# Optimization experiments

Hardware: AMD Instinct MI355X
Metric: run time of the kernel (lower is better)

Reference implementation:

```python
import jax, jax.numpy as jnp
import numpy as np


def setup_inputs() -> dict:
    key = jax.random.key(0)
    ks = jax.random.split(key, 6)
    B, T, Din, Dout = 128, 512, 256, 512
    s0 = 1.0 / np.sqrt(Din + Dout)
    s1 = 1.0 / np.sqrt(Dout + Dout)
    return {
        "x": jax.random.normal(ks[0], (B, T, Din), dtype=jnp.float32),
        "W_zr0": jax.random.normal(ks[1], (Din + Dout, 2 * Dout), dtype=jnp.float32) * s0,
        "b_zr0": jnp.zeros((2 * Dout,), dtype=jnp.float32),
        "W_h0": jax.random.normal(ks[2], (Din + Dout, Dout), dtype=jnp.float32) * s0,
        "b_h0": jnp.zeros((Dout,), dtype=jnp.float32),
        "W_zr1": jax.random.normal(ks[3], (Dout + Dout, 2 * Dout), dtype=jnp.float32) * s1,
        "b_zr1": jnp.zeros((2 * Dout,), dtype=jnp.float32),
        "W_h1": jax.random.normal(ks[4], (Dout + Dout, Dout), dtype=jnp.float32) * s1,
        "b_h1": jnp.zeros((Dout,), dtype=jnp.float32),
    }


def _gru_layer(x_seq, W_zr, b_zr, W_h, b_h):
    # x_seq: [B, T, D_in]; returns [B, T, D_out]
    hidden_dim = W_h.shape[1]

    def step(state, xt):
        ins = jnp.concatenate([xt, state], axis=-1)
        zr = jax.nn.sigmoid(ins @ W_zr + b_zr)
        z, r = jnp.split(zr, 2, axis=-1)
        cand_in = jnp.concatenate([xt, z * state], axis=-1)
        h_tmp = jnp.tanh(cand_in @ W_h + b_h)
        h = r * state + (1.0 - r) * h_tmp
        return h, h

    h0 = jnp.zeros((x_seq.shape[0], hidden_dim), dtype=x_seq.dtype)
    _, ys = jax.lax.scan(step, h0, jnp.swapaxes(x_seq, 0, 1))  # scan over time
    return jnp.swapaxes(ys, 0, 1)


def reference(x, W_zr0, b_zr0, W_h0, b_h0, W_zr1, b_zr1, W_h1, b_h1):
    h = _gru_layer(x, W_zr0, b_zr0, W_h0, b_h0)
    h = _gru_layer(h, W_zr1, b_zr1, W_h1, b_h1)
    return h
```

## Files before the change

kernel.cpp:

```cpp
#include <hip/hip_runtime.h>

#define NB 128
#define NT 512
#define DIN 256
#define DD 512

using bf16x8 = __attribute__((ext_vector_type(8))) short;
using f32x4v = __attribute__((ext_vector_type(4))) float;
using u32x4  = __attribute__((ext_vector_type(4))) unsigned int;

__device__ __forceinline__ unsigned short f2bf(float f) {
  unsigned int u = __builtin_bit_cast(unsigned int, f);
  u = (u + 0x7fffu + ((u >> 16) & 1u)) >> 16;
  return (unsigned short)u;
}
__device__ __forceinline__ float bf2f(unsigned short h) {
  unsigned int u = ((unsigned int)h) << 16;
  return __builtin_bit_cast(float, u);
}
__device__ __forceinline__ unsigned int packf(float v) {
  unsigned short hi = f2bf(v);
  unsigned short lo = f2bf(v - bf2f(hi));
  return (((unsigned int)hi) << 16) | lo;
}

__global__ void prep_kernel(const float* __restrict__ x, unsigned int* __restrict__ x_pk,
                            unsigned int* __restrict__ hp, unsigned int* __restrict__ cnt) {
  long i = (long)blockIdx.x * blockDim.x + threadIdx.x;
  const long stride = (long)gridDim.x * blockDim.x;
  const long NX = (long)NB * NT * DIN;
  for (long j = i; j < NX; j += stride) x_pk[j] = packf(x[j]);
  const long NH = 2L * 2 * NB * DD;
  for (long j = i; j < NH; j += stride) hp[j] = 0u;
  if (i < 4096) cnt[i] = 0u;
}

__device__ __forceinline__ void unpack16(const u32x4& q0, const u32x4& q1,
                                         bf16x8& hi, bf16x8& lo) {
  #pragma unroll
  for (int j = 0; j < 4; ++j) {
    hi[j]     = (short)(q0[j] >> 16);
    lo[j]     = (short)(q0[j] & 0xffffu);
    hi[4 + j] = (short)(q1[j] >> 16);
    lo[4 + j] = (short)(q1[j] & 0xffffu);
  }
}

template<int KN>
__device__ __forceinline__ void gemm_pk(const unsigned int* __restrict__ a,
                                        const unsigned short* __restrict__ b,
                                        int quad, f32x4v& cH0, f32x4v& cL0,
                                        f32x4v& cH1, f32x4v& cL1) {
  const unsigned int* ap = a + quad * 8;
  const unsigned short* bp = b + quad * 8;
  #pragma unroll
  for (int kk = 0; kk < KN; kk += 64) {
    u32x4 q0 = *(const u32x4*)(ap + kk);
    u32x4 q1 = *(const u32x4*)(ap + kk + 4);
    u32x4 q2 = *(const u32x4*)(ap + kk + 32);
    u32x4 q3 = *(const u32x4*)(ap + kk + 36);
    bf16x8 a0h, a0l, a1h, a1l;
    unpack16(q0, q1, a0h, a0l);
    unpack16(q2, q3, a1h, a1l);
    bf16x8 b0 = *(const bf16x8*)(bp + kk);
    bf16x8 b1 = *(const bf16x8*)(bp + kk + 32);
    cH0 = __builtin_amdgcn_mfma_f32_16x16x32_bf16(a0h, b0, cH0, 0, 0, 0);
    cL0 = __builtin_amdgcn_mfma_f32_16x16x32_bf16(a0l, b0, cL0, 0, 0, 0);
    cH1 = __builtin_amdgcn_mfma_f32_16x16x32_bf16(a1h, b1, cH1, 0, 0, 0);
    cL1 = __builtin_amdgcn_mfma_f32_16x16x32_bf16(a1l, b1, cL1, 0, 0, 0);
  }
}

template<int KN>
__device__ __forceinline__ void gemm_pk2(const unsigned int* __restrict__ a,
                                         const unsigned short* __restrict__ b0,
                                         const unsigned short* __restrict__ b1,
                                         int quad,
                                         f32x4v& zH0, f32x4v& zL0, f32x4v& zH1, f32x4v& zL1,
                                         f32x4v& rH0, f32x4v& rL0, f32x4v& rH1, f32x4v& rL1) {
  const unsigned int* ap = a + quad * 8;
  const unsigned short* b0p = b0 + quad * 8;
  const unsigned short* b1p = b1 + quad * 8;
  #pragma unroll
  for (int kk = 0; kk < KN; kk += 64) {
    u32x4 q0 = *(const u32x4*)(ap + kk);
    u32x4 q1 = *(const u32x4*)(ap + kk + 4);
    u32x4 q2 = *(const u32x4*)(ap + kk + 32);
    u32x4 q3 = *(const u32x4*)(ap + kk + 36);
    bf16x8 a0h, a0l, a1h, a1l;
    unpack16(q0, q1, a0h, a0l);
    unpack16(q2, q3, a1h, a1l);
    bf16x8 bz0 = *(const bf16x8*)(b0p + kk);
    bf16x8 bz1 = *(const bf16x8*)(b0p + kk + 32);
    bf16x8 br0 = *(const bf16x8*)(b1p + kk);
    bf16x8 br1 = *(const bf16x8*)(b1p + kk + 32);
    zH0 = __builtin_amdgcn_mfma_f32_16x16x32_bf16(a0h, bz0, zH0, 0, 0, 0);
    zL0 = __builtin_amdgcn_mfma_f32_16x16x32_bf16(a0l, bz0, zL0, 0, 0, 0);
    rH0 = __builtin_amdgcn_mfma_f32_16x16x32_bf16(a0h, br0, rH0, 0, 0, 0);
    rL0 = __builtin_amdgcn_mfma_f32_16x16x32_bf16(a0l, br0, rL0, 0, 0, 0);
    zH1 = __builtin_amdgcn_mfma_f32_16x16x32_bf16(a1h, bz1, zH1, 0, 0, 0);
    zL1 = __builtin_amdgcn_mfma_f32_16x16x32_bf16(a1l, bz1, zL1, 0, 0, 0);
    rH1 = __builtin_amdgcn_mfma_f32_16x16x32_bf16(a1h, br1, rH1, 0, 0, 0);
    rL1 = __builtin_amdgcn_mfma_f32_16x16x32_bf16(a1l, br1, rL1, 0, 0, 0);
  }
}

__device__ __forceinline__ void gbarrier(unsigned int* gf, int slot, int w, int lane,
                                         unsigned int rnd) {
  __syncthreads();
  if (threadIdx.x == 0)
    __hip_atomic_store(gf + slot * 16, rnd, __ATOMIC_RELAXED, __HIP_MEMORY_SCOPE_AGENT);
  if (w == 0) {
    for (;;) {
      unsigned int v = __hip_atomic_load(gf + lane * 16, __ATOMIC_RELAXED,
                                         __HIP_MEMORY_SCOPE_AGENT);
      if (__all((int)(v >= rnd))) break;
      __builtin_amdgcn_s_sleep(1);
    }
    if (lane == 0)
      (void)__hip_atomic_load(gf, __ATOMIC_ACQUIRE, __HIP_MEMORY_SCOPE_AGENT);
  }
  __syncthreads();
}

__global__ void __launch_bounds__(256, 1) gru_kernel(
    const float* __restrict__ Wzr0, const float* __restrict__ bzr0,
    const float* __restrict__ Wh0,  const float* __restrict__ bh0,
    const float* __restrict__ Wzr1, const float* __restrict__ bzr1,
    const float* __restrict__ Wh1,  const float* __restrict__ bh1,
    const unsigned int* __restrict__ x_pk, unsigned int* __restrict__ hp,
    unsigned int* __restrict__ zs, unsigned int* __restrict__ cnt,
    float* __restrict__ out)
{
  extern __shared__ __align__(16) unsigned char smem[];
  const int bid = blockIdx.x, tid = threadIdx.x;
  const int w = tid >> 6, lane = tid & 63, quad = lane >> 4, l16 = lane & 15;
  const int l  = bid >> 7;
  const int rb = (bid >> 5) & 3;
  const int cb = bid & 31;
  const int r0 = rb << 5;
  const int c0 = cb << 4;
  const int K  = l ? 1024 : 768;
  const int KI = l ? 512 : 256;
  const int ldw = K + 8;

  unsigned short* wlds = (unsigned short*)smem;
  float* s_lds = (float*)(smem + ((48 * ldw * 2 + 15) & ~15));
  float* r_lds = s_lds + 512;
  float* pscr  = r_lds + 512;

  const float* Wzr = l ? Wzr1 : Wzr0;
  const float* Wh  = l ? Wh1 : Wh0;
  for (int idx = tid; idx < 16 * K; idx += 256) {
    int j = idx / K, k = idx - j * K;
    wlds[j * ldw + k]        = f2bf(Wzr[k * (2 * DD) + c0 + j]);
    wlds[(16 + j) * ldw + k] = f2bf(Wzr[k * (2 * DD) + DD + c0 + j]);
    wlds[(32 + j) * ldw + k] = f2bf(Wh[k * DD + c0 + j]);
  }
  for (int idx = tid; idx < 512; idx += 256) s_lds[idx] = 0.f;
  const float bz = (l ? bzr1 : bzr0)[c0 + l16];
  const float br = (l ? bzr1 : bzr0)[DD + c0 + l16];
  const float bh = (l ? bh1 : bh0)[c0 + l16];
  __syncthreads();

  unsigned int* gf = cnt + rb * 1024;
  const int slot = l * 32 + cb;
  unsigned int rnd = 0;

  for (int s = 0; s <= NT; ++s) {
    const int p  = (s + 1) & 1;
    const int pw = s & 1;
    const bool act = l ? (s >= 1) : (s < NT);
    const int t = l ? (s - 1) : s;

    if (act) {
      const int rowHalf = w >> 1, seg = w & 1;
      const int gRow = r0 + (rowHalf << 4) + l16;
      f32x4v zH0 = {0,0,0,0}, zL0 = {0,0,0,0}, zH1 = {0,0,0,0}, zL1 = {0,0,0,0};
      f32x4v rH0 = {0,0,0,0}, rL0 = {0,0,0,0}, rH1 = {0,0,0,0}, rL1 = {0,0,0,0};
      const unsigned short* bzseg = wlds + l16 * ldw;
      const unsigned short* brseg = wlds + (16 + l16) * ldw;
      if (l == 0) {
        if (seg == 0) {
          const unsigned int* xa = x_pk + ((long)gRow * NT + t) * DIN;
          gemm_pk2<256>(xa, bzseg, brseg, quad, zH0, zL0, zH1, zL1, rH0, rL0, rH1, rL1);
        } else {
          const unsigned int* ha = hp + ((p * 2 + 0) * NB + gRow) * DD;
          gemm_pk2<512>(ha, bzseg + 256, brseg + 256, quad,
                        zH0, zL0, zH1, zL1, rH0, rL0, rH1, rL1);
        }
      } else {
        if (seg == 0) {
          const unsigned int* h0a = hp + ((p * 2 + 0) * NB + gRow) * DD;
          gemm_pk2<512>(h0a, bzseg, brseg, quad, zH0, zL0, zH1, zL1, rH0, rL0, rH1, rL1);
        } else {
          const unsigned int* h1a = hp + ((p * 2 + 1) * NB + gRow) * DD;
          gemm_pk2<512>(h1a, bzseg + 512, brseg + 512, quad,
                        zH0, zL0, zH1, zL1, rH0, rL0, rH1, rL1);
        }
      }
      float zt[4], rt[4];
      #pragma unroll
      for (int i = 0; i < 4; ++i) {
        zt[i] = (zH0[i] + zL0[i]) + (zH1[i] + zL1[i]);
        rt[i] = (rH0[i] + rL0[i]) + (rH1[i] + rL1[i]);
      }
      if (seg == 1) {
        #pragma unroll
        for (int i = 0; i < 4; ++i) {
          pscr[rowHalf * 512 + ((quad << 2) + i) * 16 + l16]       = zt[i];
          pscr[rowHalf * 512 + 256 + ((quad << 2) + i) * 16 + l16] = rt[i];
        }
      }
      __syncthreads();
      if (seg == 0) {
        #pragma unroll
        for (int i = 0; i < 4; ++i) {
          int rloc = (rowHalf << 4) + (quad << 2) + i;
          float zpre = zt[i] + pscr[rowHalf * 512 + ((quad << 2) + i) * 16 + l16] + bz;
          float rpre = rt[i] + pscr[rowHalf * 512 + 256 + ((quad << 2) + i) * 16 + l16] + br;
          float zg = 1.f / (1.f + __expf(-zpre));
          float rg = 1.f / (1.f + __expf(-rpre));
          float sv = s_lds[rloc * 16 + l16];
          __hip_atomic_store(&zs[((long)l * NB + r0 + rloc) * DD + c0 + l16],
                             packf(zg * sv), __ATOMIC_RELAXED, __HIP_MEMORY_SCOPE_AGENT);
          r_lds[rloc * 16 + l16] = rg;
        }
      }
    }
    ++rnd;
    gbarrier(gf, slot, w, lane, rnd);

    if (act) {
      const int rowHalf = w & 1, src = w >> 1;
      const int gRow = r0 + (rowHalf << 4) + l16;
      f32x4v cH0 = {0,0,0,0}, cL0 = {0,0,0,0}, cH1 = {0,0,0,0}, cL1 = {0,0,0,0};
      const unsigned short* hseg = wlds + (32 + l16) * ldw;
      if (src == 0) {
        if (l == 0) {
          const unsigned int* xa = x_pk + ((long)gRow * NT + t) * DIN;
          gemm_pk<256>(xa, hseg, quad, cH0, cL0, cH1, cL1);
        } else {
          const unsigned int* h0a = hp + ((p * 2 + 0) * NB + gRow) * DD;
          gemm_pk<512>(h0a, hseg, quad, cH0, cL0, cH1, cL1);
        }
      } else {
        const unsigned int* za = zs + ((long)l * NB + gRow) * DD;
        gemm_pk<512>(za, hseg + KI, quad, cH0, cL0, cH1, cL1);
      }
      f32x4v tot;
      #pragma unroll
      for (int i = 0; i < 4; ++i) tot[i] = (cH0[i] + cL0[i]) + (cH1[i] + cL1[i]);
      if (src == 1) {
        #pragma unroll
        for (int i = 0; i < 4; ++i)
          pscr[rowHalf * 256 + ((quad << 2) + i) * 16 + l16] = tot[i];
      }
      __syncthreads();
      if (src == 0) {
        #pragma unroll
        for (int i = 0; i < 4; ++i) {
          int rloc = (rowHalf << 4) + (quad << 2) + i;
          float pre = tot[i] + pscr[rowHalf * 256 + ((quad << 2) + i) * 16 + l16] + bh;
          float ax = fabsf(pre), e = __expf(-2.f * ax);
          float th = (1.f - e) / (1.f + e);
          th = (pre < 0.f) ? -th : th;
          float rv = r_lds[rloc * 16 + l16];
          float sv = s_lds[rloc * 16 + l16];
          float h = rv * sv + (1.f - rv) * th;
          s_lds[rloc * 16 + l16] = h;
          __hip_atomic_store(&hp[((pw * 2 + l) * NB + r0 + rloc) * DD + c0 + l16],
                             packf(h), __ATOMIC_RELAXED, __HIP_MEMORY_SCOPE_AGENT);
          if (l) out[((long)(r0 + rloc) * NT + t) * DD + c0 + l16] = h;
        }
      }
    }
    ++rnd;
    gbarrier(gf, slot, w, lane, rnd);
  }
}

extern "C" void kernel_launch(void* const* d_in, const int* in_sizes, int n_in,
                              void* d_out, int out_size, void* d_ws, size_t ws_size,
                              hipStream_t stream) {
  const float* x    = (const float*)d_in[0];
  const float* Wzr0 = (const float*)d_in[1];
  const float* bzr0 = (const float*)d_in[2];
  const float* Wh0  = (const float*)d_in[3];
  const float* bh0  = (const float*)d_in[4];
  const float* Wzr1 = (const float*)d_in[5];
  const float* bzr1 = (const float*)d_in[6];
  const float* Wh1  = (const float*)d_in[7];
  const float* bh1  = (const float*)d_in[8];
  float* out = (float*)d_out;

  char* pp = (char*)d_ws;
  unsigned int* cnt  = (unsigned int*)pp;  pp += 16384;
  unsigned int* x_pk = (unsigned int*)pp;  pp += (size_t)NB * NT * DIN * 4;
  unsigned int* hp   = (unsigned int*)pp;  pp += (size_t)2 * 2 * NB * DD * 4;
  unsigned int* zs   = (unsigned int*)pp;  pp += (size_t)2 * NB * DD * 4;

  hipLaunchKernelGGL(prep_kernel, dim3(1024), dim3(256), 0, stream, x, x_pk, hp, cnt);

  const int SMEM = ((48 * (1024 + 8) * 2 + 15) & ~15) + 2 * 512 * 4 + 1024 * 4;
  (void)hipFuncSetAttribute((const void*)gru_kernel,
                            hipFuncAttributeMaxDynamicSharedMemorySize, SMEM);
  hipLaunchKernelGGL(gru_kernel, dim3(256), dim3(256), SMEM, stream,
                     Wzr0, bzr0, Wh0, bh0, Wzr1, bzr1, Wh1, bh1,
                     x_pk, hp, zs, cnt, out);
}
```

Baseline: 7.554 ms.

## Double block size to 512 threads and split K across four waves per row-half

Raises the workgroup from 4 to 8 waves. Each 16-row half's K reduction for both the zr and candidate GEMMs is now split across four waves, and the partial sums are merged through a larger LDS scratch area. This is meant to shorten the per-step serial GEMM latency inside the recurrent critical path between grid barriers. The cost is more LDS reduction traffic, and the gbarrier spin now runs with twice as many threads per block. Layer 0 splits unevenly (256/192/192/128).

```diff
diff --git a/kernel.cpp b/kernel.cpp
--- a/kernel.cpp
+++ b/kernel.cpp
@@ -123,7 +123,7 @@
   __syncthreads();
 }
 
-__global__ void __launch_bounds__(256, 1) gru_kernel(
+__global__ void __launch_bounds__(512, 1) gru_kernel(
     const float* __restrict__ Wzr0, const float* __restrict__ bzr0,
     const float* __restrict__ Wh0,  const float* __restrict__ bh0,
     const float* __restrict__ Wzr1, const float* __restrict__ bzr1,
@@ -141,7 +141,6 @@
   const int r0 = rb << 5;
   const int c0 = cb << 4;
   const int K  = l ? 1024 : 768;
-  const int KI = l ? 512 : 256;
   const int ldw = K + 8;
 
   unsigned short* wlds = (unsigned short*)smem;
@@ -151,13 +150,13 @@
 
   const float* Wzr = l ? Wzr1 : Wzr0;
   const float* Wh  = l ? Wh1 : Wh0;
-  for (int idx = tid; idx < 16 * K; idx += 256) {
+  for (int idx = tid; idx < 16 * K; idx += 512) {
     int j = idx / K, k = idx - j * K;
     wlds[j * ldw + k]        = f2bf(Wzr[k * (2 * DD) + c0 + j]);
     wlds[(16 + j) * ldw + k] = f2bf(Wzr[k * (2 * DD) + DD + c0 + j]);
     wlds[(32 + j) * ldw + k] = f2bf(Wh[k * DD + c0 + j]);
   }
-  for (int idx = tid; idx < 512; idx += 256) s_lds[idx] = 0.f;
+  for (int idx = tid; idx < 512; idx += 512) s_lds[idx] = 0.f;
   const float bz = (l ? bzr1 : bzr0)[c0 + l16];
   const float br = (l ? bzr1 : bzr0)[DD + c0 + l16];
   const float bh = (l ? bh1 : bh0)[c0 + l16];
@@ -166,6 +165,10 @@
   unsigned int* gf = cnt + rb * 1024;
   const int slot = l * 32 + cb;
   unsigned int rnd = 0;
+
+  const int rowHalf = w >> 2, seg = w & 3;
+  const int gRow = r0 + (rowHalf << 4) + l16;
+  const int pidx = (quad << 2) * 16 + l16;
 
   for (int s = 0; s <= NT; ++s) {
     const int p  = (s + 1) & 1;
@@ -174,30 +177,32 @@
     const int t = l ? (s - 1) : s;
 
     if (act) {
-      const int rowHalf = w >> 1, seg = w & 1;
-      const int gRow = r0 + (rowHalf << 4) + l16;
       f32x4v zH0 = {0,0,0,0}, zL0 = {0,0,0,0}, zH1 = {0,0,0,0}, zL1 = {0,0,0,0};
       f32x4v rH0 = {0,0,0,0}, rL0 = {0,0,0,0}, rH1 = {0,0,0,0}, rL1 = {0,0,0,0};
       const unsigned short* bzseg = wlds + l16 * ldw;
       const unsigned short* brseg = wlds + (16 + l16) * ldw;
       if (l == 0) {
-        if (seg == 0) {
-          const unsigned int* xa = x_pk + ((long)gRow * NT + t) * DIN;
-          gemm_pk2<256>(xa, bzseg, brseg, quad, zH0, zL0, zH1, zL1, rH0, rL0, rH1, rL1);
-        } else {
-          const unsigned int* ha = hp + ((p * 2 + 0) * NB + gRow) * DD;
-          gemm_pk2<512>(ha, bzseg + 256, brseg + 256, quad,
-                        zH0, zL0, zH1, zL1, rH0, rL0, rH1, rL1);
-        }
+        const unsigned int* xa = x_pk + ((long)gRow * NT + t) * DIN;
+        const unsigned int* ha = hp + ((p * 2 + 0) * NB + gRow) * DD;
+        if      (seg == 0) gemm_pk2<256>(xa, bzseg, brseg, quad,
+                                         zH0, zL0, zH1, zL1, rH0, rL0, rH1, rL1);
+        else if (seg == 1) gemm_pk2<192>(ha, bzseg + 256, brseg + 256, quad,
+                                         zH0, zL0, zH1, zL1, rH0, rL0, rH1, rL1);
+        else if (seg == 2) gemm_pk2<192>(ha + 192, bzseg + 448, brseg + 448, quad,
+                                         zH0, zL0, zH1, zL1, rH0, rL0, rH1, rL1);
+        else               gemm_pk2<128>(ha + 384, bzseg + 640, brseg + 640, quad,
+                                         zH0, zL0, zH1, zL1, rH0, rL0, rH1, rL1);
       } else {
-        if (seg == 0) {
-          const unsigned int* h0a = hp + ((p * 2 + 0) * NB + gRow) * DD;
-          gemm_pk2<512>(h0a, bzseg, brseg, quad, zH0, zL0, zH1, zL1, rH0, rL0, rH1, rL1);
-        } else {
-          const unsigned int* h1a = hp + ((p * 2 + 1) * NB + gRow) * DD;
-          gemm_pk2<512>(h1a, bzseg + 512, brseg + 512, quad,
-                        zH0, zL0, zH1, zL1, rH0, rL0, rH1, rL1);
-        }
+        const unsigned int* h0a = hp + ((p * 2 + 0) * NB + gRow) * DD;
+        const unsigned int* h1a = hp + ((p * 2 + 1) * NB + gRow) * DD;
+        if      (seg == 0) gemm_pk2<256>(h0a, bzseg, brseg, quad,
+                                         zH0, zL0, zH1, zL1, rH0, rL0, rH1, rL1);
+        else if (seg == 1) gemm_pk2<256>(h0a + 256, bzseg + 256, brseg + 256, quad,
+                                         zH0, zL0, zH1, zL1, rH0, rL0, rH1, rL1);
+        else if (seg == 2) gemm_pk2<256>(h1a, bzseg + 512, brseg + 512, quad,
+                                         zH0, zL0, zH1, zL1, rH0, rL0, rH1, rL1);
+        else               gemm_pk2<256>(h1a + 256, bzseg + 768, brseg + 768, quad,
+                                         zH0, zL0, zH1, zL1, rH0, rL0, rH1, rL1);
       }
       float zt[4], rt[4];
       #pragma unroll
@@ -205,20 +210,24 @@
         zt[i] = (zH0[i] + zL0[i]) + (zH1[i] + zL1[i]);
         rt[i] = (rH0[i] + rL0[i]) + (rH1[i] + rL1[i]);
       }
-      if (seg == 1) {
+      if (seg) {
+        float* pp = pscr + rowHalf * 1536 + (seg - 1) * 512;
         #pragma unroll
         for (int i = 0; i < 4; ++i) {
-          pscr[rowHalf * 512 + ((quad << 2) + i) * 16 + l16]       = zt[i];
-          pscr[rowHalf * 512 + 256 + ((quad << 2) + i) * 16 + l16] = rt[i];
+          pp[pidx + i * 16]       = zt[i];
+          pp[256 + pidx + i * 16] = rt[i];
         }
       }
       __syncthreads();
       if (seg == 0) {
+        const float* pp = pscr + rowHalf * 1536;
         #pragma unroll
         for (int i = 0; i < 4; ++i) {
           int rloc = (rowHalf << 4) + (quad << 2) + i;
-          float zpre = zt[i] + pscr[rowHalf * 512 + ((quad << 2) + i) * 16 + l16] + bz;
-          float rpre = rt[i] + pscr[rowHalf * 512 + 256 + ((quad << 2) + i) * 16 + l16] + br;
+          float zpre = zt[i] + pp[pidx + i * 16] + pp[512 + pidx + i * 16]
+                     + pp[1024 + pidx + i * 16] + bz;
+          float rpre = rt[i] + pp[256 + pidx + i * 16] + pp[768 + pidx + i * 16]
+                     + pp[1280 + pidx + i * 16] + br;
           float zg = 1.f / (1.f + __expf(-zpre));
           float rg = 1.f / (1.f + __expf(-rpre));
           float sv = s_lds[rloc * 16 + l16];
@@ -232,36 +241,39 @@
     gbarrier(gf, slot, w, lane, rnd);
 
     if (act) {
-      const int rowHalf = w & 1, src = w >> 1;
-      const int gRow = r0 + (rowHalf << 4) + l16;
       f32x4v cH0 = {0,0,0,0}, cL0 = {0,0,0,0}, cH1 = {0,0,0,0}, cL1 = {0,0,0,0};
       const unsigned short* hseg = wlds + (32 + l16) * ldw;
-      if (src == 0) {
-        if (l == 0) {
-          const unsigned int* xa = x_pk + ((long)gRow * NT + t) * DIN;
-          gemm_pk<256>(xa, hseg, quad, cH0, cL0, cH1, cL1);
-        } else {
-          const unsigned int* h0a = hp + ((p * 2 + 0) * NB + gRow) * DD;
-          gemm_pk<512>(h0a, hseg, quad, cH0, cL0, cH1, cL1);
-        }
+      if (l == 0) {
+        const unsigned int* xa = x_pk + ((long)gRow * NT + t) * DIN;
+        const unsigned int* za = zs + ((long)l * NB + gRow) * DD;
+        if      (seg == 0) gemm_pk<256>(xa, hseg, quad, cH0, cL0, cH1, cL1);
+        else if (seg == 1) gemm_pk<192>(za, hseg + 256, quad, cH0, cL0, cH1, cL1);
+        else if (seg == 2) gemm_pk<192>(za + 192, hseg + 448, quad, cH0, cL0, cH1, cL1);
+        else               gemm_pk<128>(za + 384, hseg + 640, quad, cH0, cL0, cH1, cL1);
       } else {
+        const unsigned int* h0a = hp + ((p * 2 + 0) * NB + gRow) * DD;
         const unsigned int* za = zs + ((long)l * NB + gRow) * DD;
-        gemm_pk<512>(za, hseg + KI, quad, cH0, cL0, cH1, cL1);
+        if      (seg == 0) gemm_pk<256>(h0a, hseg, quad, cH0, cL0, cH1, cL1);
+        else if (seg == 1) gemm_pk<256>(h0a + 256, hseg + 256, quad, cH0, cL0, cH1, cL1);
+        else if (seg == 2) gemm_pk<256>(za, hseg + 512, quad, cH0, cL0, cH1, cL1);
+        else               gemm_pk<256>(za + 256, hseg + 768, quad, cH0, cL0, cH1, cL1);
       }
       f32x4v tot;
       #pragma unroll
       for (int i = 0; i < 4; ++i) tot[i] = (cH0[i] + cL0[i]) + (cH1[i] + cL1[i]);
-      if (src == 1) {
+      if (seg) {
+        float* pp = pscr + rowHalf * 768 + (seg - 1) * 256;
         #pragma unroll
-        for (int i = 0; i < 4; ++i)
-          pscr[rowHalf * 256 + ((quad << 2) + i) * 16 + l16] = tot[i];
+        for (int i = 0; i < 4; ++i) pp[pidx + i * 16] = tot[i];
       }
       __syncthreads();
-      if (src == 0) {
+      if (seg == 0) {
+        const float* pp = pscr + rowHalf * 768;
         #pragma unroll
         for (int i = 0; i < 4; ++i) {
           int rloc = (rowHalf << 4) + (quad << 2) + i;
-          float pre = tot[i] + pscr[rowHalf * 256 + ((quad << 2) + i) * 16 + l16] + bh;
+          float pre = tot[i] + pp[pidx + i * 16] + pp[256 + pidx + i * 16]
+                    + pp[512 + pidx + i * 16] + bh;
           float ax = fabsf(pre), e = __expf(-2.f * ax);
           float th = (1.f - e) / (1.f + e);
           th = (pre < 0.f) ? -th : th;
@@ -302,10 +314,10 @@
 
   hipLaunchKernelGGL(prep_kernel, dim3(1024), dim3(256), 0, stream, x, x_pk, hp, cnt);
 
-  const int SMEM = ((48 * (1024 + 8) * 2 + 15) & ~15) + 2 * 512 * 4 + 1024 * 4;
+  const int SMEM = ((48 * (1024 + 8) * 2 + 15) & ~15) + 2 * 512 * 4 + 3072 * 4;
   (void)hipFuncSetAttribute((const void*)gru_kernel,
                             hipFuncAttributeMaxDynamicSharedMemorySize, SMEM);
-  hipLaunchKernelGGL(gru_kernel, dim3(256), dim3(256), SMEM, stream,
+  hipLaunchKernelGGL(gru_kernel, dim3(256), dim3(512), SMEM, stream,
                      Wzr0, bzr0, Wh0, bh0, Wzr1, bzr1, Wh1, bh1,
                      x_pk, hp, zs, cnt, out);
 }
```

New measurement: 6.837 ms. 9.5% less time.
